# Kernel tuning notes

Hardware: AMD Instinct MI355X
Metric: run time of the kernel (lower is better)

Reference implementation:

```python
import jax, jax.numpy as jnp
import numpy as np
import math

VOCAB = 32000
EMBED = 512
B, S = 4, 2048


def setup_inputs() -> dict:
    key = jax.random.key(0)
    k1, k2, k3, k4, k5, k6 = jax.random.split(key, 6)
    x = jax.random.randint(k1, (B, S), 0, VOCAB, dtype=jnp.int64 if jax.config.jax_enable_x64 else jnp.int32)
    embed = jax.random.normal(k2, (VOCAB, EMBED), dtype=jnp.float32) * 0.02
    # torch nn.Linear stores weight as [out,in]; we keep the transposed [in,out] layout
    # so forward is x @ W + b (same math).
    qkv_w = jax.random.normal(k3, (EMBED, 3 * EMBED), dtype=jnp.float32) * (1.0 / math.sqrt(EMBED))
    qkv_b = jax.random.normal(k4, (3 * EMBED,), dtype=jnp.float32) * 0.01
    fc_w = jax.random.normal(k5, (EMBED, VOCAB), dtype=jnp.float32) * (1.0 / math.sqrt(EMBED))
    fc_b = jax.random.normal(k6, (VOCAB,), dtype=jnp.float32) * 0.01
    return {"x": x, "embed": embed, "qkv_w": qkv_w, "qkv_b": qkv_b, "fc_w": fc_w, "fc_b": fc_b}


def reference(x, embed, qkv_w, qkv_b, fc_w, fc_b):
    h = embed[x]                                   # [B,S,D] embedding lookup
    qkv = h @ qkv_w + qkv_b                        # [B,S,3D]
    Q, K, V = jnp.split(qkv, 3, axis=-1)           # each [B,S,D]
    scale = 1.0 / math.sqrt(Q.shape[-1])
    scores = jnp.einsum('bqd,bkd->bqk', Q, K) * scale   # [B,S,S]
    seq = scores.shape[-1]
    causal = jnp.tril(jnp.ones((seq, seq), dtype=bool)) # lower-triangular mask
    scores = jnp.where(causal, scores, jnp.float32(-jnp.inf))
    attn = jax.nn.softmax(scores, axis=-1)         # [B,S,S]
    out = jnp.einsum('bqk,bkd->bqd', attn, V)      # [B,S,D]
    logits = out @ fc_w + fc_b                     # [B,S,V]
    return logits
```

## Files before the change

### kernel.cpp

```cpp
#include <hip/hip_runtime.h>
#include <stdint.h>


typedef unsigned short u16;
typedef __bf16 bf16x8 __attribute__((ext_vector_type(8)));
typedef float  f32x4  __attribute__((ext_vector_type(4)));

#define MFMA_BF16(a,b,c) __builtin_amdgcn_mfma_f32_16x16x32_bf16((a),(b),(c),0,0,0)

#define NB   4
#define NS   2048
#define ND   512
#define NV   32000

__device__ __forceinline__ u16 f2bf(float f) {
  union { float f; uint32_t u; } v; v.f = f;
  uint32_t r = v.u + 0x7FFFu + ((v.u >> 16) & 1u);
  return (u16)(r >> 16);
}

__device__ __forceinline__ void gl2lds16(const void* g, void* l) {
  __builtin_amdgcn_global_load_lds(
      (__attribute__((address_space(1))) void*)(uintptr_t)g,
      (__attribute__((address_space(3))) void*)(uintptr_t)l, 16, 0, 0);
}

__global__ void k_embed(const int* __restrict__ x, const float* __restrict__ E,
                        u16* __restrict__ H) {
  int t   = blockIdx.x * 256 + threadIdx.x;
  int row = t >> 6;
  int col = (t & 63) << 3;
  int tok = x[row];
  const float4* src = (const float4*)(E + (size_t)tok * ND + col);
  float4 a = src[0], b = src[1];
  uint4 o;
  o.x = f2bf(a.x) | ((uint32_t)f2bf(a.y) << 16);
  o.y = f2bf(a.z) | ((uint32_t)f2bf(a.w) << 16);
  o.z = f2bf(b.x) | ((uint32_t)f2bf(b.y) << 16);
  o.w = f2bf(b.z) | ((uint32_t)f2bf(b.w) << 16);
  *(uint4*)(H + (size_t)t * 8) = o;
}

__global__ void k_transpose(const float* __restrict__ W, u16* __restrict__ Wt,
                            int K, int N) {
  __shared__ u16 t[64][65];
  int n0 = blockIdx.x * 64, k0 = blockIdx.y * 64;
  for (int i = threadIdx.x; i < 4096; i += 256) {
    int r = i >> 6, c = i & 63;
    t[r][c] = f2bf(W[(size_t)(k0 + r) * N + n0 + c]);
  }
  __syncthreads();
  for (int i = threadIdx.x; i < 4096; i += 256) {
    int nr = i >> 6, kc = i & 63;
    Wt[(size_t)(n0 + nr) * K + k0 + kc] = t[kc][nr];
  }
}

template <int EPI>
__global__ __launch_bounds__(256)
void k_gemm(const u16* __restrict__ A, const u16* __restrict__ Bt,
            const float* __restrict__ bias, float* __restrict__ C,
            u16* __restrict__ Qo, u16* __restrict__ Ko, u16* __restrict__ Vto,
            int N) {
  __shared__ u16 As[128 * 64];
  __shared__ u16 Bs[128 * 64];
  const int tid = threadIdx.x;
  const int w = tid >> 6, lane = tid & 63, quad = lane >> 4, l16 = lane & 15;
  const int wr = w >> 1, wc = w & 1;
  const int m0 = blockIdx.y * 128, n0 = blockIdx.x * 128;
  f32x4 acc[4][4] = {};

  for (int kt = 0; kt < 8; ++kt) {
    const int k0 = kt * 64;
#pragma unroll
    for (int it = 0; it < 4; ++it) {
      int idx = it * 256 + tid;
      int r = idx >> 3, p = idx & 7;
      gl2lds16(A + (size_t)(m0 + r) * 512 + k0 + ((p ^ (r & 7)) << 3), As + idx * 8);
    }
#pragma unroll
    for (int it = 0; it < 4; ++it) {
      int idx = it * 256 + tid;
      int r = idx >> 3, p = idx & 7;
      gl2lds16(Bt + (size_t)(n0 + r) * 512 + k0 + ((p ^ (r & 7)) << 3), Bs + idx * 8);
    }
    __syncthreads();
#pragma unroll
    for (int ks = 0; ks < 2; ++ks) {
      bf16x8 af[4], bf[4];
      const int cl = ks * 4 + quad;
#pragma unroll
      for (int mt = 0; mt < 4; ++mt) {
        int r = wr * 64 + mt * 16 + l16;
        af[mt] = *(const bf16x8*)(As + ((r * 8 + (cl ^ (r & 7))) << 3));
      }
#pragma unroll
      for (int nt = 0; nt < 4; ++nt) {
        int r = wc * 64 + nt * 16 + l16;
        bf[nt] = *(const bf16x8*)(Bs + ((r * 8 + (cl ^ (r & 7))) << 3));
      }
#pragma unroll
      for (int mt = 0; mt < 4; ++mt)
#pragma unroll
        for (int nt = 0; nt < 4; ++nt)
          acc[mt][nt] = MFMA_BF16(af[mt], bf[nt], acc[mt][nt]);
    }
    __syncthreads();
  }

#pragma unroll
  for (int nt = 0; nt < 4; ++nt) {
    const int n = n0 + wc * 64 + nt * 16 + l16;
    const float bv = bias[n];
#pragma unroll
    for (int mt = 0; mt < 4; ++mt) {
      const int mb = m0 + wr * 64 + mt * 16 + quad * 4;
#pragma unroll
      for (int j = 0; j < 4; ++j) {
        float v = acc[mt][nt][j] + bv;
        if (EPI == 0) {
          C[(size_t)(mb + j) * N + n] = v;
        } else {
          u16 hb = f2bf(v);
          int m = mb + j;
          if (n < 512)        Qo[(size_t)m * 512 + n] = hb;
          else if (n < 1024)  Ko[(size_t)m * 512 + (n - 512)] = hb;
          else {
            int d = n - 1024, bb = m >> 11, ss = m & 2047;
            Vto[((size_t)(bb * 512 + d)) * 2048 + ss] = hb;
          }
        }
      }
    }
  }
}

__global__ __launch_bounds__(256, 2)
void k_attn(const u16* __restrict__ Q, const u16* __restrict__ Kk,
            const u16* __restrict__ Vt, u16* __restrict__ O) {
  __shared__ u16 lds[64 * 512];
  u16 (*Pl)[72] = (u16(*)[72])lds;
  float* alpha_sh = (float*)(lds + 64 * 72);
  float* l_sh     = alpha_sh + 64;

  const int b = blockIdx.y, qt = blockIdx.x;
  const int tid = threadIdx.x;
  const int w = tid >> 6, lane = tid & 63, quad = lane >> 4, l16 = lane & 15;
  const int q0 = qt * 64;
  const u16* Qb = Q  + (size_t)b * NS * ND;
  const u16* Kb = Kk + (size_t)b * NS * ND;
  const u16* Vb = Vt + (size_t)b * ND * NS;
  const u16* qrow = Qb + (size_t)(q0 + w * 16 + l16) * ND + quad * 8;

  f32x4 oacc[4][8] = {};
  float m_i[4] = {-1e30f, -1e30f, -1e30f, -1e30f};
  float l_i[4] = {0.f, 0.f, 0.f, 0.f};
  const float scale = 0.044194173824159216f;

  for (int kt = 0; kt <= qt; ++kt) {
#pragma unroll
    for (int it = 0; it < 16; ++it) {
      int idx = it * 256 + tid;
      int r = idx >> 6, p = idx & 63;
      gl2lds16(Kb + (size_t)(kt * 64 + r) * ND + ((p ^ (r & 7)) << 3), lds + idx * 8);
    }
    __syncthreads();

    f32x4 s[4] = {};
#pragma unroll
    for (int ks = 0; ks < 16; ++ks) {
      bf16x8 aq = *(const bf16x8*)(qrow + ks * 32);
#pragma unroll
      for (int nt = 0; nt < 4; ++nt) {
        int r = nt * 16 + l16;
        bf16x8 bk = *(const bf16x8*)(lds + ((r * 64 + ((ks * 4 + quad) ^ (r & 7))) << 3));
        s[nt] = MFMA_BF16(aq, bk, s[nt]);
      }
    }

    const bool diag = (kt == qt);
#pragma unroll
    for (int nt = 0; nt < 4; ++nt)
#pragma unroll
      for (int j = 0; j < 4; ++j) {
        float v = s[nt][j] * scale;
        if (diag && (nt * 16 + l16) > (w * 16 + quad * 4 + j)) v = -1e30f;
        s[nt][j] = v;
      }
    float rmax[4], alj[4], rsum[4];
#pragma unroll
    for (int j = 0; j < 4; ++j)
      rmax[j] = fmaxf(fmaxf(s[0][j], s[1][j]), fmaxf(s[2][j], s[3][j]));
#pragma unroll
    for (int off = 8; off >= 1; off >>= 1)
#pragma unroll
      for (int j = 0; j < 4; ++j)
        rmax[j] = fmaxf(rmax[j], __shfl_xor(rmax[j], off));
#pragma unroll
    for (int j = 0; j < 4; ++j) {
      float mnew = fmaxf(m_i[j], rmax[j]);
      alj[j] = __expf(m_i[j] - mnew);
      m_i[j] = mnew;
    }
#pragma unroll
    for (int nt = 0; nt < 4; ++nt)
#pragma unroll
      for (int j = 0; j < 4; ++j)
        s[nt][j] = __expf(s[nt][j] - m_i[j]);
#pragma unroll
    for (int j = 0; j < 4; ++j)
      rsum[j] = (s[0][j] + s[1][j]) + (s[2][j] + s[3][j]);
#pragma unroll
    for (int off = 8; off >= 1; off >>= 1)
#pragma unroll
      for (int j = 0; j < 4; ++j)
        rsum[j] += __shfl_xor(rsum[j], off);
#pragma unroll
    for (int j = 0; j < 4; ++j)
      l_i[j] = alj[j] * l_i[j] + rsum[j];

    __syncthreads();

#pragma unroll
    for (int nt = 0; nt < 4; ++nt)
#pragma unroll
      for (int j = 0; j < 4; ++j)
        Pl[w * 16 + quad * 4 + j][nt * 16 + l16] = f2bf(s[nt][j]);
    if (l16 == 0) {
#pragma unroll
      for (int j = 0; j < 4; ++j) alpha_sh[w * 16 + quad * 4 + j] = alj[j];
    }
    __syncthreads();

#pragma unroll
    for (int mt = 0; mt < 4; ++mt)
#pragma unroll
      for (int j = 0; j < 4; ++j) {
        float al = alpha_sh[mt * 16 + quad * 4 + j];
#pragma unroll
        for (int nt = 0; nt < 8; ++nt) oacc[mt][nt][j] *= al;
      }

#pragma unroll
    for (int k2 = 0; k2 < 2; ++k2) {
      bf16x8 af[4];
#pragma unroll
      for (int mt = 0; mt < 4; ++mt)
        af[mt] = *(const bf16x8*)(&Pl[mt * 16 + l16][k2 * 32 + quad * 8]);
#pragma unroll
      for (int nt = 0; nt < 8; ++nt) {
        bf16x8 bv = *(const bf16x8*)(Vb + (size_t)(w * 128 + nt * 16 + l16) * NS +
                                     kt * 64 + k2 * 32 + quad * 8);
#pragma unroll
        for (int mt = 0; mt < 4; ++mt)
          oacc[mt][nt] = MFMA_BF16(af[mt], bv, oacc[mt][nt]);
      }
    }
    __syncthreads();
  }

  if (l16 == 0) {
#pragma unroll
    for (int j = 0; j < 4; ++j) l_sh[w * 16 + quad * 4 + j] = l_i[j];
  }
  __syncthreads();
#pragma unroll
  for (int mt = 0; mt < 4; ++mt)
#pragma unroll
    for (int j = 0; j < 4; ++j) {
      float inv = 1.0f / l_sh[mt * 16 + quad * 4 + j];
      int m = q0 + mt * 16 + quad * 4 + j;
#pragma unroll
      for (int nt = 0; nt < 8; ++nt)
        O[((size_t)b * NS + m) * ND + w * 128 + nt * 16 + l16] =
            f2bf(oacc[mt][nt][j] * inv);
    }
}

extern "C" void kernel_launch(void* const* d_in, const int* in_sizes, int n_in,
                              void* d_out, int out_size, void* d_ws, size_t ws_size,
                              hipStream_t stream) {
  (void)in_sizes; (void)n_in; (void)out_size; (void)ws_size;
  const int*   x      = (const int*)d_in[0];
  const float* embedW = (const float*)d_in[1];
  const float* qkv_w  = (const float*)d_in[2];
  const float* qkv_b  = (const float*)d_in[3];
  const float* fc_w   = (const float*)d_in[4];
  const float* fc_b   = (const float*)d_in[5];
  float* out = (float*)d_out;
  char*  ws  = (char*)d_ws;

  size_t off = 0;
  auto alloc = [&](size_t bytes) { void* p = ws + off; off += (bytes + 255) & ~(size_t)255; return p; };
  u16* Hb    = (u16*)alloc((size_t)NB * NS * ND * 2);
  u16* qkvwT = (u16*)alloc((size_t)3 * ND * ND * 2);
  u16* fcwT  = (u16*)alloc((size_t)NV * ND * 2);
  u16* Qp    = (u16*)alloc((size_t)NB * NS * ND * 2);
  u16* Kp    = (u16*)alloc((size_t)NB * NS * ND * 2);
  u16* Vtp   = (u16*)alloc((size_t)NB * ND * NS * 2);
  u16* Ob    = (u16*)alloc((size_t)NB * NS * ND * 2);

  k_transpose<<<dim3(1536 / 64, 512 / 64), 256, 0, stream>>>(qkv_w, qkvwT, 512, 1536);
  k_transpose<<<dim3(NV / 64, 512 / 64), 256, 0, stream>>>(fc_w, fcwT, 512, NV);
  k_embed<<<(NB * NS * 64) / 256, 256, 0, stream>>>(x, embedW, Hb);
  k_gemm<1><<<dim3(1536 / 128, (NB * NS) / 128), 256, 0, stream>>>(
      Hb, qkvwT, qkv_b, nullptr, Qp, Kp, Vtp, 1536);
  k_attn<<<dim3(NS / 64, NB), 256, 0, stream>>>(Qp, Kp, Vtp, Ob);
  k_gemm<0><<<dim3(NV / 128, (NB * NS) / 128), 256, 0, stream>>>(
      Ob, fcwT, fc_b, out, nullptr, nullptr, nullptr, NV);
}
```

Before: 1.922 ms.

## Use 256x256-tile double-buffered GEMM with grouped block ordering for output projection

Replaces the 128x128-tile output-projection GEMM with a new 512-thread kernel using 256x256 tiles, XOR-swizzled LDS staging via direct global-to-LDS loads, and double buffering across the K loop. Block IDs are remapped into grouped super-tiles so that concurrently running blocks share A and B panels in L2. The aim is higher arithmetic intensity and better cache reuse for the largest GEMM. In exchange it uses 128KB of LDS per block, which limits occupancy, and it hardcodes a tile-mapping formula specific to these shapes.

```diff
diff --git a/kernel.cpp b/kernel.cpp
--- a/kernel.cpp
+++ b/kernel.cpp
@@ -135,6 +135,106 @@
   }
 }
 
+__device__ __forceinline__ void stage_tile256(const u16* __restrict__ A,
+                                              const u16* __restrict__ Bt,
+                                              int m0, int n0, int k0,
+                                              u16* As, u16* Bs, int tid) {
+#pragma unroll
+  for (int it = 0; it < 4; ++it) {
+    int idx = it * 512 + tid;
+    int r = idx >> 3, p = idx & 7;
+    gl2lds16(A + (size_t)(m0 + r) * 512 + k0 + ((p ^ (r & 7)) << 3), As + idx * 8);
+  }
+#pragma unroll
+  for (int it = 0; it < 4; ++it) {
+    int idx = it * 512 + tid;
+    int r = idx >> 3, p = idx & 7;
+    gl2lds16(Bt + (size_t)(n0 + r) * 512 + k0 + ((p ^ (r & 7)) << 3), Bs + idx * 8);
+  }
+}
+
+__global__ __launch_bounds__(512, 2)
+void k_gemm256(const u16* __restrict__ A, const u16* __restrict__ Bt,
+               const float* __restrict__ bias, float* __restrict__ C, int N) {
+  __shared__ u16 As[2][256 * 64];
+  __shared__ u16 Bs[2][256 * 64];
+  const int tid = threadIdx.x;
+  const int w = tid >> 6, lane = tid & 63, quad = lane >> 4, l16 = lane & 15;
+  const int wr = w >> 2, wc = w & 3;
+
+  const int bid = blockIdx.x;
+  const int l  = (bid & 7) * 500 + (bid >> 3);
+  const int st = l / 40, si = l % 40;
+  const int m0 = ((st & 3) * 8 + (si & 7)) * 256;
+  const int n0 = ((st >> 2) * 5 + (si >> 3)) * 256;
+
+  f32x4 acc[8][4] = {};
+
+  stage_tile256(A, Bt, m0, n0, 0, As[0], Bs[0], tid);
+  int cur = 0;
+  for (int t = 0; t < 8; ++t) {
+    if (t < 7) {
+      stage_tile256(A, Bt, m0, n0, (t + 1) * 64, As[cur ^ 1], Bs[cur ^ 1], tid);
+      asm volatile("s_waitcnt vmcnt(8)" ::: "memory");
+    } else {
+      asm volatile("s_waitcnt vmcnt(0)" ::: "memory");
+    }
+    __builtin_amdgcn_s_barrier();
+    __builtin_amdgcn_sched_barrier(0);
+
+    const u16* Ab = As[cur];
+    const u16* Bb = Bs[cur];
+    bf16x8 bfr[4][2];
+#pragma unroll
+    for (int nt = 0; nt < 4; ++nt)
+#pragma unroll
+      for (int kk = 0; kk < 2; ++kk) {
+        int r = wc * 64 + nt * 16 + l16;
+        int cl = kk * 4 + quad;
+        bfr[nt][kk] = *(const bf16x8*)(Bb + ((r * 8 + (cl ^ (r & 7))) << 3));
+      }
+#pragma unroll
+    for (int qd = 0; qd < 4; ++qd) {
+      bf16x8 af[2][2];
+#pragma unroll
+      for (int mi = 0; mi < 2; ++mi)
+#pragma unroll
+        for (int kk = 0; kk < 2; ++kk) {
+          int r = wr * 128 + (qd * 2 + mi) * 16 + l16;
+          int cl = kk * 4 + quad;
+          af[mi][kk] = *(const bf16x8*)(Ab + ((r * 8 + (cl ^ (r & 7))) << 3));
+        }
+      __builtin_amdgcn_s_setprio(1);
+#pragma unroll
+      for (int mi = 0; mi < 2; ++mi)
+#pragma unroll
+        for (int nt = 0; nt < 4; ++nt)
+#pragma unroll
+          for (int kk = 0; kk < 2; ++kk)
+            acc[qd * 2 + mi][nt] =
+                MFMA_BF16(af[mi][kk], bfr[nt][kk], acc[qd * 2 + mi][nt]);
+      __builtin_amdgcn_s_setprio(0);
+    }
+    asm volatile("" ::: "memory");
+    __builtin_amdgcn_s_barrier();
+    __builtin_amdgcn_sched_barrier(0);
+    cur ^= 1;
+  }
+
+#pragma unroll
+  for (int nt = 0; nt < 4; ++nt) {
+    const int n = n0 + wc * 64 + nt * 16 + l16;
+    const float bv = bias[n];
+#pragma unroll
+    for (int mt = 0; mt < 8; ++mt) {
+      const int mb = m0 + wr * 128 + mt * 16 + quad * 4;
+#pragma unroll
+      for (int j = 0; j < 4; ++j)
+        C[(size_t)(mb + j) * N + n] = acc[mt][nt][j] + bv;
+    }
+  }
+}
+
 __global__ __launch_bounds__(256, 2)
 void k_attn(const u16* __restrict__ Q, const u16* __restrict__ Kk,
             const u16* __restrict__ Vt, u16* __restrict__ O) {
@@ -306,6 +406,6 @@
   k_gemm<1><<<dim3(1536 / 128, (NB * NS) / 128), 256, 0, stream>>>(
       Hb, qkvwT, qkv_b, nullptr, Qp, Kp, Vtp, 1536);
   k_attn<<<dim3(NS / 64, NB), 256, 0, stream>>>(Qp, Kp, Vtp, Ob);
-  k_gemm<0><<<dim3(NV / 128, (NB * NS) / 128), 256, 0, stream>>>(
-      Ob, fcwT, fc_b, out, nullptr, nullptr, nullptr, NV);
-}
+  k_gemm256<<<dim3((NV / 256) * ((NB * NS) / 256)), 512, 0, stream>>>(
+      Ob, fcwT, fc_b, out, NV);
+}
```

New measurement: 1.872 ms. 2.6% less time.
